# Kernel optimization log

Hardware: AMD Instinct MI355X
Metric: run time of the kernel (lower is better)

## Reference

```python
import jax, jax.numpy as jnp
import numpy as np

D_K = 64
SCALE = 1.0 / (D_K ** 0.5)
NEG_INF = float('-inf')


def setup_inputs() -> dict:
    key = jax.random.key(0)
    kq, kk, kv = jax.random.split(key, 3)
    B, H, S, D = 2, 16, 2048, D_K
    Q = jax.random.normal(kq, (B, H, S, D), dtype=jnp.float32)
    K = jax.random.normal(kk, (B, H, S, D), dtype=jnp.float32)
    V = jax.random.normal(kv, (B, H, S, D), dtype=jnp.float32)
    # causal mask: True = attend, False = masked (matches masked_fill(mask == False, -inf))
    mask = jnp.tril(jnp.ones((S, S), dtype=jnp.bool_))
    return {"Q": Q, "K": K, "V": V, "mask": mask}


def reference(Q, K, V, mask):
    # scores: [B, H, q, k]
    scores = jnp.einsum('bhqd,bhkd->bhqk', Q, K) * SCALE
    scores = jnp.where(mask, scores, NEG_INF)
    # hand-rolled stable softmax, same math as the torch module
    x_exp = jnp.exp(scores - jnp.max(scores, axis=-1, keepdims=True))
    attn = x_exp / jnp.sum(x_exp, axis=-1, keepdims=True)
    out = jnp.einsum('bhqk,bhkv->bhqv', attn, V)
    return out
```

## Files before the change

kernel.cpp:

```cpp
#include <hip/hip_runtime.h>
#include <hip/hip_bf16.h>

#define S_LEN   2048
#define D_DIM   64
#define BK      64
#define NBH     32

typedef __attribute__((ext_vector_type(8))) short  short8;
typedef __attribute__((ext_vector_type(4))) float  floatx4;

#define KLD   72
#define VTLD  72
#define PLD   72
#define OLD   65

#define VOFF  9216
#define POFF  18432
#define SMEM_BYTES 36864

__device__ __forceinline__ unsigned pk2(float lo, float hi) {
  __hip_bfloat162 h = __float22bfloat162_rn(float2{lo, hi});
  union { __hip_bfloat162 v; unsigned u; } c; c.v = h;
  return c.u;
}
__device__ __forceinline__ short8 pk8(const float* f) {
  union { short8 s; unsigned u[4]; } r;
  r.u[0] = pk2(f[0], f[1]); r.u[1] = pk2(f[2], f[3]);
  r.u[2] = pk2(f[4], f[5]); r.u[3] = pk2(f[6], f[7]);
  return r.s;
}
__device__ __forceinline__ float bf2f(unsigned short s) {
  union { unsigned u; float f; } c; c.u = ((unsigned)s) << 16; return c.f;
}

__device__ const unsigned char SCH_QI [24] = {7,15,13,14,14,12,12,11, 15,13,6,10,8,8,10,11, 0,1,2,3,4,5,9,9};
__device__ const unsigned char SCH_SPL[24] = {0,1,1,1,1,1,1,1,       1,1,0,1,1,1,1,1,      0,0,0,0,0,0,1,1};
__device__ const unsigned char SCH_HLF[24] = {0,1,1,0,1,0,1,0,       0,0,0,0,0,1,1,1,      0,0,0,0,0,0,0,1};

__global__ __launch_bounds__(256, 2)
void fa_fwd(const float* __restrict__ Qg,
            const float* __restrict__ Kg,
            const float* __restrict__ Vg,
            float* __restrict__ Og,
            unsigned short* __restrict__ Opart,
            float* __restrict__ Lpart)
{
  __shared__ char smem[SMEM_BYTES];
  short* Klds  = (short*)smem;
  short* Vtlds = (short*)(smem + VOFF);

  const int tid  = threadIdx.x;
  const int wv   = tid >> 6;
  const int lane = tid & 63;
  const int col  = lane & 15;
  const int quad = lane >> 4;
  short* PA = (short*)(smem + POFF) + wv * (32 * PLD);
  short* PB = PA + 16 * PLD;
  float* Olds = (float*)smem + wv * (16 * OLD);

  const int b   = (int)blockIdx.x;
  const int idx = ((b >> 8) << 3) | ((b >> 5) & 7);
  const int bh  = b & 31;
  const int qi  = SCH_QI[idx];
  const bool split = SCH_SPL[idx] != 0;
  const int half  = SCH_HLF[idx];
  int it0, itend;
  {
    const int nk = 2 * (qi + 1);
    if (split) { it0 = half ? (qi + 1) : 0; itend = half ? nk : (qi + 1); }
    else       { it0 = 0;                   itend = nk; }
  }
  const int q0 = qi * 128;

  const float qscale = 0.18033688011112042f;
  const float* Qb = Qg + (size_t)bh * S_LEN * D_DIM;
  const float* Kb = Kg + (size_t)bh * S_LEN * D_DIM;
  const float* Vb = Vg + (size_t)bh * S_LEN * D_DIM;
  float*       Ob = Og + (size_t)bh * S_LEN * D_DIM;

  const int srow = tid >> 2;
  const int sseg = (tid & 3) * 16;
  const int kp2  = tid & 31;
  const int dg   = (tid >> 5) * 8;

  const int qws[2] = {q0 + wv * 16, q0 + 64 + wv * 16};

  short8 qf[2][2];
#pragma unroll
  for (int qt = 0; qt < 2; ++qt)
#pragma unroll
    for (int h = 0; h < 2; ++h) {
      const float* qp = Qb + (size_t)(qws[qt] + col) * D_DIM + h * 32 + quad * 8;
      union { float4 v[2]; float f[8]; } u;
      u.v[0] = *(const float4*)qp; u.v[1] = *(const float4*)(qp + 4);
      float t[8];
#pragma unroll
      for (int j = 0; j < 8; ++j) t[j] = u.f[j] * qscale;
      qf[qt][h] = pk8(t);
    }

  floatx4 o[2][4];
#pragma unroll
  for (int qt = 0; qt < 2; ++qt)
#pragma unroll
    for (int dt = 0; dt < 4; ++dt) o[qt][dt] = (floatx4){0.f,0.f,0.f,0.f};
  float l_run[2] = {0.f, 0.f};

  union f16u { float4 v[4]; float f[16]; };
  f16u kpre, vpre;
  {
    const float* kp = Kb + (size_t)(it0 * BK + srow) * D_DIM + sseg;
    kpre.v[0] = *(const float4*)kp;       kpre.v[1] = *(const float4*)(kp + 4);
    kpre.v[2] = *(const float4*)(kp + 8); kpre.v[3] = *(const float4*)(kp + 12);
    const float* vp = Vb + (size_t)(it0 * BK + 2 * kp2) * D_DIM + dg;
    vpre.v[0] = *(const float4*)vp;             vpre.v[1] = *(const float4*)(vp + 4);
    vpre.v[2] = *(const float4*)(vp + D_DIM);   vpre.v[3] = *(const float4*)(vp + D_DIM + 4);
  }

  for (int it = it0; it < itend; ++it) {
    __syncthreads();
    *(short8*)&Klds[srow * KLD + sseg]     = pk8(kpre.f);
    *(short8*)&Klds[srow * KLD + sseg + 8] = pk8(kpre.f + 8);
#pragma unroll
    for (int i = 0; i < 8; ++i)
      *(unsigned*)&Vtlds[(dg + i) * VTLD + 2 * kp2] = pk2(vpre.f[i], vpre.f[8 + i]);
    __syncthreads();

    if (it + 1 < itend) {
      const int kb2 = (it + 1) * BK;
      const float* kp = Kb + (size_t)(kb2 + srow) * D_DIM + sseg;
      kpre.v[0] = *(const float4*)kp;       kpre.v[1] = *(const float4*)(kp + 4);
      kpre.v[2] = *(const float4*)(kp + 8); kpre.v[3] = *(const float4*)(kp + 12);
      const float* vp = Vb + (size_t)(kb2 + 2 * kp2) * D_DIM + dg;
      vpre.v[0] = *(const float4*)vp;             vpre.v[1] = *(const float4*)(vp + 4);
      vpre.v[2] = *(const float4*)(vp + D_DIM);   vpre.v[3] = *(const float4*)(vp + D_DIM + 4);
    }

    const int  kb  = it * BK;
    const bool doA = (kb != q0 + 64);

    floatx4 st[2][4];
#pragma unroll
    for (int kt = 0; kt < 4; ++kt) {
      short8 kf0 = *(short8*)&Klds[(kt * 16 + col) * KLD + quad * 8];
      short8 kf1 = *(short8*)&Klds[(kt * 16 + col) * KLD + 32 + quad * 8];
      floatx4 c = (floatx4){0.f,0.f,0.f,0.f};
      c = __builtin_amdgcn_mfma_f32_16x16x32_bf16(kf0, qf[1][0], c, 0, 0, 0);
      c = __builtin_amdgcn_mfma_f32_16x16x32_bf16(kf1, qf[1][1], c, 0, 0, 0);
      st[1][kt] = c;
      if (doA) {
        floatx4 d = (floatx4){0.f,0.f,0.f,0.f};
        d = __builtin_amdgcn_mfma_f32_16x16x32_bf16(kf0, qf[0][0], d, 0, 0, 0);
        d = __builtin_amdgcn_mfma_f32_16x16x32_bf16(kf1, qf[0][1], d, 0, 0, 0);
        st[0][kt] = d;
      }
    }

    if (kb == q0) {
      const int qg = qws[0] + col;
#pragma unroll
      for (int kt = 0; kt < 4; ++kt)
#pragma unroll
        for (int r = 0; r < 4; ++r)
          if (kb + kt * 16 + quad * 4 + r > qg) st[0][kt][r] = -3.0e38f;
    }
    if (!doA) {
      const int qg = qws[1] + col;
#pragma unroll
      for (int kt = 0; kt < 4; ++kt)
#pragma unroll
        for (int r = 0; r < 4; ++r)
          if (kb + kt * 16 + quad * 4 + r > qg) st[1][kt][r] = -3.0e38f;
    }

#pragma unroll
    for (int qt = 0; qt < 2; ++qt) {
      if (qt == 0 && !doA) continue;
      float lsum = 0.f;
#pragma unroll
      for (int kt = 0; kt < 4; ++kt)
#pragma unroll
        for (int r = 0; r < 4; ++r) {
          const float p = __builtin_amdgcn_exp2f(st[qt][kt][r]);
          st[qt][kt][r] = p;
          lsum += p;
        }
      l_run[qt] += lsum;
      short* Pq = qt ? PB : PA;
#pragma unroll
      for (int kt = 0; kt < 4; ++kt) {
        uint2 w; w.x = pk2(st[qt][kt][0], st[qt][kt][1]); w.y = pk2(st[qt][kt][2], st[qt][kt][3]);
        *(uint2*)&Pq[col * PLD + kt * 16 + quad * 4] = w;
      }
    }

#pragma unroll
    for (int g = 0; g < 2; ++g) {
      short8 pfB = *(short8*)&PB[col * PLD + g * 32 + quad * 8];
      short8 pfA;
      if (doA) pfA = *(short8*)&PA[col * PLD + g * 32 + quad * 8];
#pragma unroll
      for (int dt = 0; dt < 4; ++dt) {
        short8 vf = *(short8*)&Vtlds[(dt * 16 + col) * VTLD + g * 32 + quad * 8];
        o[1][dt] = __builtin_amdgcn_mfma_f32_16x16x32_bf16(vf, pfB, o[1][dt], 0, 0, 0);
        if (doA)
          o[0][dt] = __builtin_amdgcn_mfma_f32_16x16x32_bf16(vf, pfA, o[0][dt], 0, 0, 0);
      }
    }
  }

  __syncthreads();
#pragma unroll
  for (int qt = 0; qt < 2; ++qt) {
    float l = l_run[qt];
    l += __shfl_xor(l, 16);
    l += __shfl_xor(l, 32);
    if (!split) {
      const float inv = 1.0f / l;
#pragma unroll
      for (int dt = 0; dt < 4; ++dt)
#pragma unroll
        for (int r = 0; r < 4; ++r)
          Olds[col * OLD + dt * 16 + quad * 4 + r] = o[qt][dt][r] * inv;
#pragma unroll
      for (int it2 = 0; it2 < 4; ++it2) {
        const int ql = it2 * 4 + quad;
        float4 w;
        w.x = Olds[ql * OLD + col * 4 + 0];
        w.y = Olds[ql * OLD + col * 4 + 1];
        w.z = Olds[ql * OLD + col * 4 + 2];
        w.w = Olds[ql * OLD + col * 4 + 3];
        *(float4*)(Ob + (size_t)(qws[qt] + ql) * D_DIM + col * 4) = w;
      }
    } else {
#pragma unroll
      for (int dt = 0; dt < 4; ++dt)
#pragma unroll
        for (int r = 0; r < 4; ++r)
          Olds[col * OLD + dt * 16 + quad * 4 + r] = o[qt][dt][r];
#pragma unroll
      for (int it2 = 0; it2 < 4; ++it2) {
        const int ql = it2 * 4 + quad;
        const int p  = qws[qt] + ql - 1024;
        float4 w;
        w.x = Olds[ql * OLD + col * 4 + 0];
        w.y = Olds[ql * OLD + col * 4 + 1];
        w.z = Olds[ql * OLD + col * 4 + 2];
        w.w = Olds[ql * OLD + col * 4 + 3];
        uint2 pw; pw.x = pk2(w.x, w.y); pw.y = pk2(w.z, w.w);
        *(uint2*)&Opart[((size_t)(half * 32 + bh) * 1024 + p) * 64 + col * 4] = pw;
      }
      if (quad == 0)
        Lpart[(half * 32 + bh) * 1024 + (qws[qt] + col - 1024)] = l;
    }
  }
}

__global__ __launch_bounds__(256, 2)
void merge(const unsigned short* __restrict__ Opart,
           const float* __restrict__ Lpart,
           float* __restrict__ Og)
{
  const int tid = threadIdx.x;
  const int gid = blockIdx.x * 64 + (tid >> 2);
  const int seg = (tid & 3) * 16;
  const int bh  = gid >> 10;
  const int p   = gid & 1023;
  const float la = Lpart[(0 * 32 + bh) * 1024 + p];
  const float lb = Lpart[(1 * 32 + bh) * 1024 + p];
  const float inv = 1.0f / (la + lb);
  const unsigned short* pa = Opart + ((size_t)(0 * 32 + bh) * 1024 + p) * 64 + seg;
  const unsigned short* pb = Opart + ((size_t)(1 * 32 + bh) * 1024 + p) * 64 + seg;
  union { short8 s; unsigned short h[8]; } a0, a1, b0, b1;
  a0.s = *(short8*)pa; a1.s = *(short8*)(pa + 8);
  b0.s = *(short8*)pb; b1.s = *(short8*)(pb + 8);
  float out[16];
#pragma unroll
  for (int j = 0; j < 8; ++j) out[j]     = (bf2f(a0.h[j]) + bf2f(b0.h[j])) * inv;
#pragma unroll
  for (int j = 0; j < 8; ++j) out[8 + j] = (bf2f(a1.h[j]) + bf2f(b1.h[j])) * inv;
  float* dst = Og + ((size_t)bh * S_LEN + 1024 + p) * D_DIM + seg;
#pragma unroll
  for (int j = 0; j < 4; ++j)
    *(float4*)(dst + 4 * j) = *(float4*)&out[4 * j];
}

extern "C" void kernel_launch(void* const* d_in, const int* in_sizes, int n_in,
                              void* d_out, int out_size, void* d_ws, size_t ws_size,
                              hipStream_t stream) {
  const float* Q = (const float*)d_in[0];
  const float* K = (const float*)d_in[1];
  const float* V = (const float*)d_in[2];
  float* O = (float*)d_out;
  unsigned short* Opart = (unsigned short*)d_ws;
  float*          Lpart = (float*)(Opart + (size_t)2 * 32 * 1024 * 64);

  hipLaunchKernelGGL(fa_fwd, dim3(768), dim3(256), 0, stream, Q, K, V, O, Opart, Lpart);
  hipLaunchKernelGGL(merge,  dim3(512), dim3(256), 0, stream, Opart, Lpart, O);
}
```

Measured before the change: 133.7 us.

## Double-buffer K/V tiles in LDS with XOR swizzle and one barrier per iteration

```diff
diff --git a/kernel.cpp b/kernel.cpp
--- a/kernel.cpp
+++ b/kernel.cpp
@@ -9,14 +9,14 @@
 typedef __attribute__((ext_vector_type(8))) short  short8;
 typedef __attribute__((ext_vector_type(4))) float  floatx4;
 
-#define KLD   72
-#define VTLD  72
-#define PLD   72
-#define OLD   65
-
-#define VOFF  9216
-#define POFF  18432
-#define SMEM_BYTES 36864
+#define VBUF0   16384
+#define PBASE   32768
+#define SMEM_BYTES 49152
+#define OLD     65
+
+__device__ __forceinline__ char* swz(char* base, int row, int byte) {
+  return base + row * 128 + (byte ^ ((row & 7) << 4));
+}
 
 __device__ __forceinline__ unsigned pk2(float lo, float hi) {
   __hip_bfloat162 h = __float22bfloat162_rn(float2{lo, hi});
@@ -46,16 +46,13 @@
             float* __restrict__ Lpart)
 {
   __shared__ char smem[SMEM_BYTES];
-  short* Klds  = (short*)smem;
-  short* Vtlds = (short*)(smem + VOFF);
 
   const int tid  = threadIdx.x;
   const int wv   = tid >> 6;
   const int lane = tid & 63;
   const int col  = lane & 15;
   const int quad = lane >> 4;
-  short* PA = (short*)(smem + POFF) + wv * (32 * PLD);
-  short* PB = PA + 16 * PLD;
+  char* Pw = smem + PBASE + (wv << 12);
   float* Olds = (float*)smem + wv * (16 * OLD);
 
   const int b   = (int)blockIdx.x;
@@ -79,7 +76,7 @@
   float*       Ob = Og + (size_t)bh * S_LEN * D_DIM;
 
   const int srow = tid >> 2;
-  const int sseg = (tid & 3) * 16;
+  const int sb   = (tid & 3) * 32;
   const int kp2  = tid & 31;
   const int dg   = (tid >> 5) * 8;
 
@@ -109,7 +106,7 @@
   union f16u { float4 v[4]; float f[16]; };
   f16u kpre, vpre;
   {
-    const float* kp = Kb + (size_t)(it0 * BK + srow) * D_DIM + sseg;
+    const float* kp = Kb + (size_t)(it0 * BK + srow) * D_DIM + sb / 2;
     kpre.v[0] = *(const float4*)kp;       kpre.v[1] = *(const float4*)(kp + 4);
     kpre.v[2] = *(const float4*)(kp + 8); kpre.v[3] = *(const float4*)(kp + 12);
     const float* vp = Vb + (size_t)(it0 * BK + 2 * kp2) * D_DIM + dg;
@@ -117,18 +114,23 @@
     vpre.v[2] = *(const float4*)(vp + D_DIM);   vpre.v[3] = *(const float4*)(vp + D_DIM + 4);
   }
 
+  {
+    char* Kst = smem;
+    char* Vst = smem + VBUF0;
+    *(short8*)swz(Kst, srow, sb)      = pk8(kpre.f);
+    *(short8*)swz(Kst, srow, sb + 16) = pk8(kpre.f + 8);
+#pragma unroll
+    for (int i = 0; i < 8; ++i)
+      *(unsigned*)swz(Vst, dg + i, kp2 * 4) = pk2(vpre.f[i], vpre.f[8 + i]);
+  }
+  __syncthreads();
+
+  int cur = 0;
   for (int it = it0; it < itend; ++it) {
-    __syncthreads();
-    *(short8*)&Klds[srow * KLD + sseg]     = pk8(kpre.f);
-    *(short8*)&Klds[srow * KLD + sseg + 8] = pk8(kpre.f + 8);
-#pragma unroll
-    for (int i = 0; i < 8; ++i)
-      *(unsigned*)&Vtlds[(dg + i) * VTLD + 2 * kp2] = pk2(vpre.f[i], vpre.f[8 + i]);
-    __syncthreads();
-
-    if (it + 1 < itend) {
+    const bool more = (it + 1 < itend);
+    if (more) {
       const int kb2 = (it + 1) * BK;
-      const float* kp = Kb + (size_t)(kb2 + srow) * D_DIM + sseg;
+      const float* kp = Kb + (size_t)(kb2 + srow) * D_DIM + sb / 2;
       kpre.v[0] = *(const float4*)kp;       kpre.v[1] = *(const float4*)(kp + 4);
       kpre.v[2] = *(const float4*)(kp + 8); kpre.v[3] = *(const float4*)(kp + 12);
       const float* vp = Vb + (size_t)(kb2 + 2 * kp2) * D_DIM + dg;
@@ -136,14 +138,17 @@
       vpre.v[2] = *(const float4*)(vp + D_DIM);   vpre.v[3] = *(const float4*)(vp + D_DIM + 4);
     }
 
+    char* Kc = smem + (cur << 13);
+    char* Vc = smem + VBUF0 + (cur << 13);
+
     const int  kb  = it * BK;
     const bool doA = (kb != q0 + 64);
 
     floatx4 st[2][4];
 #pragma unroll
     for (int kt = 0; kt < 4; ++kt) {
-      short8 kf0 = *(short8*)&Klds[(kt * 16 + col) * KLD + quad * 8];
-      short8 kf1 = *(short8*)&Klds[(kt * 16 + col) * KLD + 32 + quad * 8];
+      short8 kf0 = *(const short8*)swz(Kc, kt * 16 + col, quad * 16);
+      short8 kf1 = *(const short8*)swz(Kc, kt * 16 + col, 64 + quad * 16);
       floatx4 c = (floatx4){0.f,0.f,0.f,0.f};
       c = __builtin_amdgcn_mfma_f32_16x16x32_bf16(kf0, qf[1][0], c, 0, 0, 0);
       c = __builtin_amdgcn_mfma_f32_16x16x32_bf16(kf1, qf[1][1], c, 0, 0, 0);
@@ -186,30 +191,41 @@
           lsum += p;
         }
       l_run[qt] += lsum;
-      short* Pq = qt ? PB : PA;
 #pragma unroll
       for (int kt = 0; kt < 4; ++kt) {
         uint2 w; w.x = pk2(st[qt][kt][0], st[qt][kt][1]); w.y = pk2(st[qt][kt][2], st[qt][kt][3]);
-        *(uint2*)&Pq[col * PLD + kt * 16 + quad * 4] = w;
-      }
+        *(uint2*)swz(Pw, qt * 16 + col, kt * 32 + quad * 8) = w;
+      }
+    }
+
+    if (more) {
+      char* Kst = smem + ((cur ^ 1) << 13);
+      char* Vst = smem + VBUF0 + ((cur ^ 1) << 13);
+      *(short8*)swz(Kst, srow, sb)      = pk8(kpre.f);
+      *(short8*)swz(Kst, srow, sb + 16) = pk8(kpre.f + 8);
+#pragma unroll
+      for (int i = 0; i < 8; ++i)
+        *(unsigned*)swz(Vst, dg + i, kp2 * 4) = pk2(vpre.f[i], vpre.f[8 + i]);
     }
 
 #pragma unroll
     for (int g = 0; g < 2; ++g) {
-      short8 pfB = *(short8*)&PB[col * PLD + g * 32 + quad * 8];
+      short8 pfB = *(const short8*)swz(Pw, 16 + col, g * 64 + quad * 16);
       short8 pfA;
-      if (doA) pfA = *(short8*)&PA[col * PLD + g * 32 + quad * 8];
+      if (doA) pfA = *(const short8*)swz(Pw, col, g * 64 + quad * 16);
 #pragma unroll
       for (int dt = 0; dt < 4; ++dt) {
-        short8 vf = *(short8*)&Vtlds[(dt * 16 + col) * VTLD + g * 32 + quad * 8];
+        short8 vf = *(const short8*)swz(Vc, dt * 16 + col, g * 64 + quad * 16);
         o[1][dt] = __builtin_amdgcn_mfma_f32_16x16x32_bf16(vf, pfB, o[1][dt], 0, 0, 0);
         if (doA)
           o[0][dt] = __builtin_amdgcn_mfma_f32_16x16x32_bf16(vf, pfA, o[0][dt], 0, 0, 0);
       }
     }
-  }
-
-  __syncthreads();
+
+    __syncthreads();
+    cur ^= 1;
+  }
+
 #pragma unroll
   for (int qt = 0; qt < 2; ++qt) {
     float l = l_run[qt];
```

New measurement: 153.9 us. +15.1%, slower.
